# Performance work log

Hardware: AMD Instinct MI355X
Metric: run time of the kernel (lower is better)

The kernel has to match this reference:

```python
import jax, jax.numpy as jnp
import numpy as np

B, L, D, H = 4, 2048, 1024, 16
DH = D // H

def setup_inputs() -> dict:
    key = jax.random.key(0)
    ks = jax.random.split(key, 9)
    s = 1.0 / np.sqrt(D)
    x = jax.random.normal(ks[0], (B, L, D), dtype=jnp.float32)
    Wq = jax.random.uniform(ks[1], (D, D), jnp.float32, -s, s)
    bq = jax.random.uniform(ks[2], (D,), jnp.float32, -s, s)
    Wk = jax.random.uniform(ks[3], (D, D), jnp.float32, -s, s)
    bk = jax.random.uniform(ks[4], (D,), jnp.float32, -s, s)
    Wv = jax.random.uniform(ks[5], (D, D), jnp.float32, -s, s)
    bv = jax.random.uniform(ks[6], (D,), jnp.float32, -s, s)
    Wo = jax.random.uniform(ks[7], (D, D), jnp.float32, -s, s)
    bo = jax.random.uniform(ks[8], (D,), jnp.float32, -s, s)
    mask = jnp.tril(jnp.ones((L, L), dtype=jnp.int32))[None, None]  # [1,1,L,L] causal
    return {"x": x, "Wq": Wq, "bq": bq, "Wk": Wk, "bk": bk, "Wv": Wv, "bv": bv,
            "Wo": Wo, "bo": bo, "mask": mask}

def reference(x, Wq, bq, Wk, bk, Wv, bv, Wo, bo, mask):
    # projections (torch Linear: x @ W.T + b; here W stored transposed already as [D,D])
    q = (x @ Wq + bq).reshape(B, L, H, DH).transpose(0, 2, 1, 3)  # [B,H,L,Dh]
    k = (x @ Wk + bk).reshape(B, L, H, DH).transpose(0, 2, 1, 3)
    v = (x @ Wv + bv).reshape(B, L, H, DH).transpose(0, 2, 1, 3)
    scores = jnp.einsum('bhqd,bhkd->bhqk', q, k) / jnp.sqrt(jnp.float32(DH))
    scores = jnp.where(mask == 0, -jnp.inf, scores)
    attn = jax.nn.softmax(scores, axis=-1)
    out = jnp.einsum('bhqk,bhkd->bhqd', attn, v)  # [B,H,L,Dh]
    out = out.transpose(0, 2, 1, 3).reshape(B, L, D)
    return out @ Wo + bo
```

## Files before the change

kernel.cpp:

```cpp
#include <hip/hip_runtime.h>
#include <hip/hip_bf16.h>


typedef __bf16 bf16;
typedef __bf16 bf16x4 __attribute__((ext_vector_type(4)));
typedef __bf16 bf16x8 __attribute__((ext_vector_type(8)));
typedef float f32x4 __attribute__((ext_vector_type(4)));

#define DEV static __device__ __forceinline__

constexpr int B = 4, L = 2048, D = 1024, H = 16, DH = 64;
constexpr int BL = B * L;
constexpr int GM = 8192, GK = 1024;
constexpr int BKg = 64;

typedef __attribute__((address_space(1))) const void* gptr1;
typedef __attribute__((address_space(3))) void* lptr3;

DEV void load_lds16(const bf16* g, bf16* l) {
  __builtin_amdgcn_global_load_lds((gptr1)g, (lptr3)l, 16, 0, 0);
}

DEV f32x4 mfma(bf16x8 a, bf16x8 b, f32x4 c) {
  return __builtin_amdgcn_mfma_f32_16x16x32_bf16(a, b, c, 0, 0, 0);
}

DEV float scrub(float v) { return (v == v) ? v : 0.f; }
DEV float max3f(float a, float b, float c) { return fmaxf(fmaxf(a, b), c); }

__global__ void sniff_k(const unsigned short* __restrict__ xr, int* flag) {
  __shared__ int cnt;
  if (threadIdx.x == 0) cnt = 0;
  __syncthreads();
  int local = 0;
  for (int i = threadIdx.x; i < 4096; i += 256) {
    const unsigned short u = xr[2 * i];
    const int e = (u >> 7) & 0xFF;
    if (e >= 0x70 && e <= 0x85) local++;
  }
  atomicAdd(&cnt, local);
  __syncthreads();
  if (threadIdx.x == 0) *flag = (cnt > 2048) ? 1 : 0;
}

__global__ __launch_bounds__(256) void cvt_x_k(const void* __restrict__ src,
                                               bf16* __restrict__ dst,
                                               const int* __restrict__ flag, int n) {
  const bool isbf = (*flag != 0);
  const int stride = gridDim.x * blockDim.x * 8;
  for (int idx = (blockIdx.x * blockDim.x + threadIdx.x) * 8; idx < n; idx += stride) {
    bf16x8 o;
    if (isbf) {
      bf16x8 v = *(const bf16x8*)((const bf16*)src + idx);
      #pragma unroll
      for (int j = 0; j < 8; ++j) o[j] = (bf16)scrub((float)v[j]);
    } else {
      const float* s = (const float*)src + idx;
      #pragma unroll
      for (int j = 0; j < 8; ++j) o[j] = (bf16)scrub(s[j]);
    }
    *(bf16x8*)&dst[idx] = o;
  }
}

__global__ __launch_bounds__(256) void wtrans_cvt4_k(const void* __restrict__ W0,
                                                     const void* __restrict__ W1,
                                                     const void* __restrict__ W2,
                                                     const void* __restrict__ W3,
                                                     bf16* __restrict__ dstBase,
                                                     const int* __restrict__ flag) {
  __shared__ bf16 t[32][33];
  const bool isbf = (*flag != 0);
  const int z = blockIdx.z;
  const void* src = (z == 0) ? W0 : (z == 1) ? W1 : (z == 2) ? W2 : W3;
  bf16* dst = dstBase + (size_t)z * D * D;
  const int bx = blockIdx.x * 32, by = blockIdx.y * 32;
  const int tx = threadIdx.x & 31, ty = threadIdx.x >> 5;
  for (int i = ty; i < 32; i += 8) {
    const size_t off = (size_t)(by + i) * D + bx + tx;
    const float v = isbf ? (float)((const bf16*)src)[off] : ((const float*)src)[off];
    t[i][tx] = (bf16)scrub(v);
  }
  __syncthreads();
  for (int i = ty; i < 32; i += 8)
    dst[(size_t)(bx + i) * D + by + tx] = t[tx][i];
}

__global__ __launch_bounds__(256) void qkv_gemm_k(const bf16* __restrict__ A,
                                                  const bf16* __restrict__ Bt,
                                                  const void* __restrict__ bq,
                                                  const void* __restrict__ bk,
                                                  const void* __restrict__ bv,
                                                  bf16* __restrict__ Q,
                                                  bf16* __restrict__ Kk,
                                                  bf16* __restrict__ VT,
                                                  const int* __restrict__ flag) {
  __shared__ __align__(16) bf16 As[128 * BKg];
  __shared__ __align__(16) bf16 Bs[128 * BKg];
  const bool isbf = (*flag != 0);
  const int wg = blockIdx.x;
  const int local = wg >> 3;
  const int mt = (wg & 7) * 8 + (local & 7);
  const int nt = local >> 3;
  const int m0 = mt * 128, n0 = nt * 128;
  const int buf = n0 >> 10, nloc = n0 & 1023;
  const void* bias = (buf == 0) ? bq : (buf == 1) ? bk : bv;
  const float scale = (buf == 0) ? 0.18033688011111f : 1.0f;

  const int tid = threadIdx.x, wave = tid >> 6, lane = tid & 63;
  const int wr = wave >> 1, wc = wave & 1;
  const int quad = lane >> 4, l16 = lane & 15;
  const int srow = lane >> 3;
  const int scol = ((lane ^ srow) & 7) * 8;
  const int l7 = l16 & 7;
  const int s0 = ((quad ^ l7) * 8);
  const int s1 = s0 ^ 32;

  f32x4 acc[4][4] = {};

  for (int k0 = 0; k0 < GK; k0 += BKg) {
    for (int c = wave; c < 16; c += 4) {
      load_lds16(A  + (size_t)(m0 + c * 8 + srow) * GK + k0 + scol, &As[c * 512]);
      load_lds16(Bt + (size_t)(n0 + c * 8 + srow) * GK + k0 + scol, &Bs[c * 512]);
    }
    __syncthreads();
    #pragma unroll
    for (int kk = 0; kk < BKg; kk += 32) {
      const int sk = kk ? s1 : s0;
      bf16x8 af[4], bfr[4];
      #pragma unroll
      for (int i = 0; i < 4; ++i)
        af[i] = *(const bf16x8*)&As[(wr * 64 + i * 16 + l16) * BKg + sk];
      #pragma unroll
      for (int i = 0; i < 4; ++i)
        bfr[i] = *(const bf16x8*)&Bs[(wc * 64 + i * 16 + l16) * BKg + sk];
      #pragma unroll
      for (int mi = 0; mi < 4; ++mi)
        #pragma unroll
        for (int ni = 0; ni < 4; ++ni)
          acc[mi][ni] = mfma(af[mi], bfr[ni], acc[mi][ni]);
    }
    __syncthreads();
  }

  if (buf < 2) {
    bf16* Cb = (buf == 0) ? Q : Kk;
    #pragma unroll
    for (int ni = 0; ni < 4; ++ni) {
      const int col = nloc + wc * 64 + ni * 16 + l16;
      const float bv2 = isbf ? (float)((const bf16*)bias)[col] : ((const float*)bias)[col];
      #pragma unroll
      for (int mi = 0; mi < 4; ++mi)
        #pragma unroll
        for (int r = 0; r < 4; ++r) {
          const int row = m0 + wr * 64 + mi * 16 + quad * 4 + r;
          Cb[(size_t)row * D + col] = (bf16)((acc[mi][ni][r] + bv2) * scale);
        }
    }
  } else {
    #pragma unroll
    for (int ni = 0; ni < 4; ++ni) {
      const int col = nloc + wc * 64 + ni * 16 + l16;
      const int h = col >> 6, d = col & 63;
      const float bv2 = isbf ? (float)((const bf16*)bias)[col] : ((const float*)bias)[col];
      #pragma unroll
      for (int mi = 0; mi < 4; ++mi) {
        const int row = m0 + wr * 64 + mi * 16 + quad * 4;
        const int bb = row >> 11, l = row & 2047;
        const int pos = (l & ~31) + 4 * ((l >> 4) & 1) + 8 * ((l >> 2) & 3);
        bf16x4 pk;
        #pragma unroll
        for (int r = 0; r < 4; ++r) pk[r] = (bf16)(acc[mi][ni][r] + bv2);
        *(bf16x4*)&VT[((size_t)(bb * 16 + h) * 64 + d) * L + pos] = pk;
      }
    }
  }
}

__global__ __launch_bounds__(256) void gemm_bt_k(const bf16* __restrict__ A,
                                                 const bf16* __restrict__ Bt,
                                                 const void* __restrict__ bias,
                                                 void* __restrict__ C,
                                                 const int* __restrict__ flag) {
  __shared__ __align__(16) bf16 As[128 * BKg];
  __shared__ __align__(16) bf16 Bs[128 * BKg];
  const bool isbf = (*flag != 0);
  const int wg = blockIdx.x;
  const int local = wg >> 3;
  const int mt = (wg & 7) * 8 + (local & 7);
  const int nt = local >> 3;
  const int m0 = mt * 128, n0 = nt * 128;
  const int tid = threadIdx.x, wave = tid >> 6, lane = tid & 63;
  const int wr = wave >> 1, wc = wave & 1;
  const int quad = lane >> 4, l16 = lane & 15;
  const int srow = lane >> 3;
  const int scol = ((lane ^ srow) & 7) * 8;
  const int l7 = l16 & 7;
  const int s0 = ((quad ^ l7) * 8);
  const int s1 = s0 ^ 32;

  f32x4 acc[4][4] = {};

  for (int k0 = 0; k0 < GK; k0 += BKg) {
    for (int c = wave; c < 16; c += 4) {
      load_lds16(A  + (size_t)(m0 + c * 8 + srow) * GK + k0 + scol, &As[c * 512]);
      load_lds16(Bt + (size_t)(n0 + c * 8 + srow) * GK + k0 + scol, &Bs[c * 512]);
    }
    __syncthreads();
    #pragma unroll
    for (int kk = 0; kk < BKg; kk += 32) {
      const int sk = kk ? s1 : s0;
      bf16x8 af[4], bfr[4];
      #pragma unroll
      for (int i = 0; i < 4; ++i)
        af[i] = *(const bf16x8*)&As[(wr * 64 + i * 16 + l16) * BKg + sk];
      #pragma unroll
      for (int i = 0; i < 4; ++i)
        bfr[i] = *(const bf16x8*)&Bs[(wc * 64 + i * 16 + l16) * BKg + sk];
      #pragma unroll
      for (int mi = 0; mi < 4; ++mi)
        #pragma unroll
        for (int ni = 0; ni < 4; ++ni)
          acc[mi][ni] = mfma(af[mi], bfr[ni], acc[mi][ni]);
    }
    __syncthreads();
  }

  bf16* Cb = (bf16*)C;
  float* Cf = (float*)C;
  #pragma unroll
  for (int ni = 0; ni < 4; ++ni) {
    const int col = n0 + wc * 64 + ni * 16 + l16;
    const float bv = isbf ? (float)((const bf16*)bias)[col] : ((const float*)bias)[col];
    #pragma unroll
    for (int mi = 0; mi < 4; ++mi)
      #pragma unroll
      for (int r = 0; r < 4; ++r) {
        const int row = m0 + wr * 64 + mi * 16 + quad * 4 + r;
        const float v = acc[mi][ni][r] + bv;
        if (isbf) Cb[(size_t)row * D + col] = (bf16)v;
        else      Cf[(size_t)row * D + col] = v;
      }
  }
}

__global__ __launch_bounds__(256) void attn_k(bf16* QO,
                                              const bf16* __restrict__ K,
                                              const bf16* __restrict__ VT) {
  __shared__ __align__(16) bf16 Ks[2][64 * 64];
  __shared__ __align__(16) bf16 Vt[2][64 * 64];

  const int bx = blockIdx.x;
  const int qt = (L / 64 - 1) - (bx >> 6);
  const int bh = bx & 63;
  const int b = bh >> 4, h = bh & 15;
  const int tid = threadIdx.x, wave = tid >> 6, lane = tid & 63;
  const int quad = lane >> 4, l16 = lane & 15;
  const int srow = lane >> 3;
  const int scol = ((lane ^ srow) & 7) * 8;
  const int l7 = l16 & 7;
  const int s0 = ((quad ^ l7) * 8);
  const int s1 = s0 ^ 32;

  bf16* Qb = QO + (size_t)b * L * D + h * DH;
  const bf16* Kb = K + (size_t)b * L * D + h * DH;
  const bf16* VTg = VT + (size_t)bh * DH * L;

  const int qrow = qt * 64 + wave * 16 + l16;
  const bf16x8 qf0 = *(const bf16x8*)(Qb + (size_t)qrow * D + quad * 8);
  const bf16x8 qf1 = *(const bf16x8*)(Qb + (size_t)qrow * D + 32 + quad * 8);

  bf16x8 ones;
  #pragma unroll
  for (int j = 0; j < 8; ++j) ones[j] = (bf16)1.0f;

  float m_run = -INFINITY;
  f32x4 o_acc[4] = {};
  f32x4 o_sum = {};

  const int nkt = qt + 1;

  const bf16* kg0 = Kb + (size_t)(wave * 8 + srow) * D + scol;
  const bf16* kg1 = kg0 + (size_t)32 * D;
  const bf16* vg0 = VTg + (size_t)(wave * 8 + srow) * L + scol;
  const bf16* vg1 = vg0 + (size_t)32 * L;
  const int kl0 = wave * 512, kl1 = kl0 + 2048;

  load_lds16(kg0, &Ks[0][kl0]);
  load_lds16(kg1, &Ks[0][kl1]);
  load_lds16(vg0, &Vt[0][kl0]);
  load_lds16(vg1, &Vt[0][kl1]);
  kg0 += (size_t)64 * D; kg1 += (size_t)64 * D; vg0 += 64; vg1 += 64;
  __syncthreads();

  int cur = 0;
  for (int kt = 0; kt < nkt; ++kt) {
    if (kt + 1 < nkt) {
      bf16* Kn = &Ks[cur ^ 1][0];
      bf16* Vn = &Vt[cur ^ 1][0];
      load_lds16(kg0, &Kn[kl0]);
      load_lds16(kg1, &Kn[kl1]);
      load_lds16(vg0, &Vn[kl0]);
      load_lds16(vg1, &Vn[kl1]);
      kg0 += (size_t)64 * D; kg1 += (size_t)64 * D; vg0 += 64; vg1 += 64;
    }

    const bf16* Kc = &Ks[cur][0];
    const bf16* Vc = &Vt[cur][0];

    f32x4 s[4];
    #pragma unroll
    for (int sub = 0; sub < 4; ++sub) {
      bf16x8 k0 = *(const bf16x8*)&Kc[(sub * 16 + l16) * 64 + s0];
      bf16x8 k1 = *(const bf16x8*)&Kc[(sub * 16 + l16) * 64 + s1];
      f32x4 a = {};
      a = mfma(k0, qf0, a);
      a = mfma(k1, qf1, a);
      s[sub] = a;
    }

    if (kt == qt) {
      const int qloc = wave * 16 + l16;
      #pragma unroll
      for (int sub = 0; sub < 4; ++sub)
        #pragma unroll
        for (int r = 0; r < 4; ++r)
          if (sub * 16 + quad * 4 + r > qloc) s[sub][r] = -1e30f;
    }

    const float t0 = max3f(s[0][0], s[0][1], s[0][2]);
    const float t1 = max3f(s[0][3], s[1][0], s[1][1]);
    const float t2 = max3f(s[1][2], s[1][3], s[2][0]);
    const float t3 = max3f(s[2][1], s[2][2], s[2][3]);
    const float t4 = max3f(s[3][0], s[3][1], s[3][2]);
    float mx = fmaxf(max3f(t0, t1, t2), max3f(t3, t4, s[3][3]));
    mx = fmaxf(mx, __shfl_xor(mx, 16, 64));
    mx = fmaxf(mx, __shfl_xor(mx, 32, 64));

    if (!__all(mx <= m_run + 8.f)) {
      const float mn = fmaxf(m_run, mx);
      const float alpha = __builtin_amdgcn_exp2f(m_run - mn);
      m_run = mn;
      #pragma unroll
      for (int r = 0; r < 4; ++r) {
        const float ar = __shfl(alpha, quad * 4 + r, 64);
        o_sum[r] *= ar;
        #pragma unroll
        for (int db = 0; db < 4; ++db) o_acc[db][r] *= ar;
      }
    }

    bf16x8 fr0, fr1;
    #pragma unroll
    for (int r = 0; r < 4; ++r) {
      fr0[r]     = (bf16)__builtin_amdgcn_exp2f(s[0][r] - m_run);
      fr0[4 + r] = (bf16)__builtin_amdgcn_exp2f(s[1][r] - m_run);
      fr1[r]     = (bf16)__builtin_amdgcn_exp2f(s[2][r] - m_run);
      fr1[4 + r] = (bf16)__builtin_amdgcn_exp2f(s[3][r] - m_run);
    }

    o_sum = mfma(fr0, ones, o_sum);
    o_sum = mfma(fr1, ones, o_sum);
    #pragma unroll
    for (int db = 0; db < 4; ++db) {
      bf16x8 v0 = *(const bf16x8*)&Vc[(db * 16 + l16) * 64 + s0];
      bf16x8 v1 = *(const bf16x8*)&Vc[(db * 16 + l16) * 64 + s1];
      o_acc[db] = mfma(fr0, v0, o_acc[db]);
      o_acc[db] = mfma(fr1, v1, o_acc[db]);
    }

    __syncthreads();
    cur ^= 1;
  }

  #pragma unroll
  for (int r = 0; r < 4; ++r) {
    const float inv = 1.f / o_sum[r];
    const int row = qt * 64 + wave * 16 + quad * 4 + r;
    #pragma unroll
    for (int db = 0; db < 4; ++db)
      Qb[(size_t)row * D + db * 16 + l16] = (bf16)(o_acc[db][r] * inv);
  }
}

extern "C" void kernel_launch(void* const* d_in, const int* in_sizes, int n_in,
                              void* d_out, int out_size, void* d_ws, size_t ws_size,
                              hipStream_t stream) {
  const void* x  = d_in[0];
  const void* Wq = d_in[1];
  const void* bq = d_in[2];
  const void* Wk = d_in[3];
  const void* bk = d_in[4];
  const void* Wv = d_in[5];
  const void* bv = d_in[6];
  const void* Wo = d_in[7];
  const void* bo = d_in[8];

  int* flag = (int*)d_ws;
  char* p = (char*)d_ws + 4096;
  bf16* xc  = (bf16*)p;                 p += (size_t)BL * D * 2;
  bf16* WqT = (bf16*)p;                 p += (size_t)D * D * 2;
  bf16* WkT = (bf16*)p;                 p += (size_t)D * D * 2;
  bf16* WvT = (bf16*)p;                 p += (size_t)D * D * 2;
  bf16* WoT = (bf16*)p;                 p += (size_t)D * D * 2;
  bf16* Qb  = (bf16*)p;                 p += (size_t)BL * D * 2;
  bf16* Kb  = (bf16*)p;                 p += (size_t)BL * D * 2;
  bf16* VTb = (bf16*)p;

  sniff_k<<<1, 256, 0, stream>>>((const unsigned short*)x, flag);

  cvt_x_k<<<1024, 256, 0, stream>>>(x, xc, flag, BL * D);
  wtrans_cvt4_k<<<dim3(32, 32, 4), 256, 0, stream>>>(Wq, Wk, Wv, Wo, WqT, flag);

  qkv_gemm_k<<<dim3(1536), 256, 0, stream>>>(
      xc, WqT, bq, bk, bv, Qb, Kb, VTb, flag);

  attn_k<<<dim3((L / 64) * B * H), 256, 0, stream>>>(Qb, Kb, VTb);

  gemm_bt_k<<<dim3(512), 256, 0, stream>>>(Qb, WoT, bo, d_out, flag);
}
```

Measured before the change: 267.6 us.

## Process two query tiles per attention block and simplify GEMM grid mapping

The attention kernel now handles 128 query rows per block as two 64-row sub-tiles. Each K/V tile is loaded into LDS once and reused for both sub-tiles, which halves K/V traffic per query and doubles MFMA work between barriers. The trade-off is more registers per thread and fewer blocks, so the causal load imbalance between blocks gets coarser. The GEMM kernels also drop the swizzled 1D block-to-tile mapping in favour of a plain 2D grid, which may reduce L2 locality.

```diff
diff --git a/kernel.cpp b/kernel.cpp
--- a/kernel.cpp
+++ b/kernel.cpp
@@ -98,11 +98,7 @@
   __shared__ __align__(16) bf16 As[128 * BKg];
   __shared__ __align__(16) bf16 Bs[128 * BKg];
   const bool isbf = (*flag != 0);
-  const int wg = blockIdx.x;
-  const int local = wg >> 3;
-  const int mt = (wg & 7) * 8 + (local & 7);
-  const int nt = local >> 3;
-  const int m0 = mt * 128, n0 = nt * 128;
+  const int m0 = blockIdx.x * 128, n0 = blockIdx.y * 128;
   const int buf = n0 >> 10, nloc = n0 & 1023;
   const void* bias = (buf == 0) ? bq : (buf == 1) ? bk : bv;
   const float scale = (buf == 0) ? 0.18033688011111f : 1.0f;
@@ -185,11 +181,7 @@
   __shared__ __align__(16) bf16 As[128 * BKg];
   __shared__ __align__(16) bf16 Bs[128 * BKg];
   const bool isbf = (*flag != 0);
-  const int wg = blockIdx.x;
-  const int local = wg >> 3;
-  const int mt = (wg & 7) * 8 + (local & 7);
-  const int nt = local >> 3;
-  const int m0 = mt * 128, n0 = nt * 128;
+  const int m0 = blockIdx.x * 128, n0 = blockIdx.y * 128;
   const int tid = threadIdx.x, wave = tid >> 6, lane = tid & 63;
   const int wr = wave >> 1, wc = wave & 1;
   const int quad = lane >> 4, l16 = lane & 15;
@@ -251,7 +243,7 @@
   __shared__ __align__(16) bf16 Vt[2][64 * 64];
 
   const int bx = blockIdx.x;
-  const int qt = (L / 64 - 1) - (bx >> 6);
+  const int qt = (L / 128 - 1) - (bx >> 6);
   const int bh = bx & 63;
   const int b = bh >> 4, h = bh & 15;
   const int tid = threadIdx.x, wave = tid >> 6, lane = tid & 63;
@@ -266,19 +258,23 @@
   const bf16* Kb = K + (size_t)b * L * D + h * DH;
   const bf16* VTg = VT + (size_t)bh * DH * L;
 
-  const int qrow = qt * 64 + wave * 16 + l16;
-  const bf16x8 qf0 = *(const bf16x8*)(Qb + (size_t)qrow * D + quad * 8);
-  const bf16x8 qf1 = *(const bf16x8*)(Qb + (size_t)qrow * D + 32 + quad * 8);
+  bf16x8 qf[2][2];
+  #pragma unroll
+  for (int sq = 0; sq < 2; ++sq) {
+    const int qrow = qt * 128 + sq * 64 + wave * 16 + l16;
+    qf[sq][0] = *(const bf16x8*)(Qb + (size_t)qrow * D + quad * 8);
+    qf[sq][1] = *(const bf16x8*)(Qb + (size_t)qrow * D + 32 + quad * 8);
+  }
 
   bf16x8 ones;
   #pragma unroll
   for (int j = 0; j < 8; ++j) ones[j] = (bf16)1.0f;
 
-  float m_run = -INFINITY;
-  f32x4 o_acc[4] = {};
-  f32x4 o_sum = {};
-
-  const int nkt = qt + 1;
+  float m_run[2] = {-INFINITY, -INFINITY};
+  f32x4 o_acc[2][4] = {};
+  f32x4 o_sum[2] = {};
+
+  const int nkt = 2 * qt + 2;
 
   const bf16* kg0 = Kb + (size_t)(wave * 8 + srow) * D + scol;
   const bf16* kg1 = kg0 + (size_t)32 * D;
@@ -308,65 +304,78 @@
     const bf16* Kc = &Ks[cur][0];
     const bf16* Vc = &Vt[cur][0];
 
-    f32x4 s[4];
+    bf16x8 kf0[4], kf1[4];
     #pragma unroll
     for (int sub = 0; sub < 4; ++sub) {
-      bf16x8 k0 = *(const bf16x8*)&Kc[(sub * 16 + l16) * 64 + s0];
-      bf16x8 k1 = *(const bf16x8*)&Kc[(sub * 16 + l16) * 64 + s1];
-      f32x4 a = {};
-      a = mfma(k0, qf0, a);
-      a = mfma(k1, qf1, a);
-      s[sub] = a;
-    }
-
-    if (kt == qt) {
-      const int qloc = wave * 16 + l16;
-      #pragma unroll
-      for (int sub = 0; sub < 4; ++sub)
-        #pragma unroll
-        for (int r = 0; r < 4; ++r)
-          if (sub * 16 + quad * 4 + r > qloc) s[sub][r] = -1e30f;
-    }
-
-    const float t0 = max3f(s[0][0], s[0][1], s[0][2]);
-    const float t1 = max3f(s[0][3], s[1][0], s[1][1]);
-    const float t2 = max3f(s[1][2], s[1][3], s[2][0]);
-    const float t3 = max3f(s[2][1], s[2][2], s[2][3]);
-    const float t4 = max3f(s[3][0], s[3][1], s[3][2]);
-    float mx = fmaxf(max3f(t0, t1, t2), max3f(t3, t4, s[3][3]));
-    mx = fmaxf(mx, __shfl_xor(mx, 16, 64));
-    mx = fmaxf(mx, __shfl_xor(mx, 32, 64));
-
-    if (!__all(mx <= m_run + 8.f)) {
-      const float mn = fmaxf(m_run, mx);
-      const float alpha = __builtin_amdgcn_exp2f(m_run - mn);
-      m_run = mn;
+      kf0[sub] = *(const bf16x8*)&Kc[(sub * 16 + l16) * 64 + s0];
+      kf1[sub] = *(const bf16x8*)&Kc[(sub * 16 + l16) * 64 + s1];
+    }
+
+    f32x4 sv[2][4];
+    #pragma unroll
+    for (int sq = 0; sq < 2; ++sq)
+      #pragma unroll
+      for (int sub = 0; sub < 4; ++sub) {
+        f32x4 a = {};
+        a = mfma(kf0[sub], qf[sq][0], a);
+        a = mfma(kf1[sub], qf[sq][1], a);
+        sv[sq][sub] = a;
+      }
+
+    bf16x8 fr[2][2];
+    #pragma unroll
+    for (int sq = 0; sq < 2; ++sq) {
+      if (kt >= 2 * qt + sq) {
+        const int qloc = (2 * qt + sq - kt) * 64 + wave * 16 + l16;
+        #pragma unroll
+        for (int sub = 0; sub < 4; ++sub)
+          #pragma unroll
+          for (int r = 0; r < 4; ++r)
+            if (sub * 16 + quad * 4 + r > qloc) sv[sq][sub][r] = -1e30f;
+      }
+
+      const float t0 = max3f(sv[sq][0][0], sv[sq][0][1], sv[sq][0][2]);
+      const float t1 = max3f(sv[sq][0][3], sv[sq][1][0], sv[sq][1][1]);
+      const float t2 = max3f(sv[sq][1][2], sv[sq][1][3], sv[sq][2][0]);
+      const float t3 = max3f(sv[sq][2][1], sv[sq][2][2], sv[sq][2][3]);
+      const float t4 = max3f(sv[sq][3][0], sv[sq][3][1], sv[sq][3][2]);
+      float mx = fmaxf(max3f(t0, t1, t2), max3f(t3, t4, sv[sq][3][3]));
+      mx = fmaxf(mx, __shfl_xor(mx, 16, 64));
+      mx = fmaxf(mx, __shfl_xor(mx, 32, 64));
+
+      if (!__all(mx <= m_run[sq] + 8.f)) {
+        const float mn = fmaxf(m_run[sq], mx);
+        const float alpha = __builtin_amdgcn_exp2f(m_run[sq] - mn);
+        m_run[sq] = mn;
+        #pragma unroll
+        for (int r = 0; r < 4; ++r) {
+          const float ar = __shfl(alpha, quad * 4 + r, 64);
+          o_sum[sq][r] *= ar;
+          #pragma unroll
+          for (int db = 0; db < 4; ++db) o_acc[sq][db][r] *= ar;
+        }
+      }
+
       #pragma unroll
       for (int r = 0; r < 4; ++r) {
-        const float ar = __shfl(alpha, quad * 4 + r, 64);
-        o_sum[r] *= ar;
-        #pragma unroll
-        for (int db = 0; db < 4; ++db) o_acc[db][r] *= ar;
-      }
-    }
-
-    bf16x8 fr0, fr1;
-    #pragma unroll
-    for (int r = 0; r < 4; ++r) {
-      fr0[r]     = (bf16)__builtin_amdgcn_exp2f(s[0][r] - m_run);
-      fr0[4 + r] = (bf16)__builtin_amdgcn_exp2f(s[1][r] - m_run);
-      fr1[r]     = (bf16)__builtin_amdgcn_exp2f(s[2][r] - m_run);
-      fr1[4 + r] = (bf16)__builtin_amdgcn_exp2f(s[3][r] - m_run);
-    }
-
-    o_sum = mfma(fr0, ones, o_sum);
-    o_sum = mfma(fr1, ones, o_sum);
+        fr[sq][0][r]     = (bf16)__builtin_amdgcn_exp2f(sv[sq][0][r] - m_run[sq]);
+        fr[sq][0][4 + r] = (bf16)__builtin_amdgcn_exp2f(sv[sq][1][r] - m_run[sq]);
+        fr[sq][1][r]     = (bf16)__builtin_amdgcn_exp2f(sv[sq][2][r] - m_run[sq]);
+        fr[sq][1][4 + r] = (bf16)__builtin_amdgcn_exp2f(sv[sq][3][r] - m_run[sq]);
+      }
+
+      o_sum[sq] = mfma(fr[sq][0], ones, o_sum[sq]);
+      o_sum[sq] = mfma(fr[sq][1], ones, o_sum[sq]);
+    }
+
     #pragma unroll
     for (int db = 0; db < 4; ++db) {
       bf16x8 v0 = *(const bf16x8*)&Vc[(db * 16 + l16) * 64 + s0];
       bf16x8 v1 = *(const bf16x8*)&Vc[(db * 16 + l16) * 64 + s1];
-      o_acc[db] = mfma(fr0, v0, o_acc[db]);
-      o_acc[db] = mfma(fr1, v1, o_acc[db]);
+      o_acc[0][db] = mfma(fr[0][0], v0, o_acc[0][db]);
+      o_acc[0][db] = mfma(fr[0][1], v1, o_acc[0][db]);
+      o_acc[1][db] = mfma(fr[1][0], v0, o_acc[1][db]);
+      o_acc[1][db] = mfma(fr[1][1], v1, o_acc[1][db]);
     }
 
     __syncthreads();
@@ -374,13 +383,15 @@
   }
 
   #pragma unroll
-  for (int r = 0; r < 4; ++r) {
-    const float inv = 1.f / o_sum[r];
-    const int row = qt * 64 + wave * 16 + quad * 4 + r;
-    #pragma unroll
-    for (int db = 0; db < 4; ++db)
-      Qb[(size_t)row * D + db * 16 + l16] = (bf16)(o_acc[db][r] * inv);
-  }
+  for (int sq = 0; sq < 2; ++sq)
+    #pragma unroll
+    for (int r = 0; r < 4; ++r) {
+      const float inv = 1.f / o_sum[sq][r];
+      const int row = qt * 128 + sq * 64 + wave * 16 + quad * 4 + r;
+      #pragma unroll
+      for (int db = 0; db < 4; ++db)
+        Qb[(size_t)row * D + db * 16 + l16] = (bf16)(o_acc[sq][db][r] * inv);
+    }
 }
 
 extern "C" void kernel_launch(void* const* d_in, const int* in_sizes, int n_in,
@@ -412,10 +423,10 @@
   cvt_x_k<<<1024, 256, 0, stream>>>(x, xc, flag, BL * D);
   wtrans_cvt4_k<<<dim3(32, 32, 4), 256, 0, stream>>>(Wq, Wk, Wv, Wo, WqT, flag);
 
-  qkv_gemm_k<<<dim3(1536), 256, 0, stream>>>(
+  qkv_gemm_k<<<dim3(GM / 128, 3072 / 128), 256, 0, stream>>>(
       xc, WqT, bq, bk, bv, Qb, Kb, VTb, flag);
 
-  attn_k<<<dim3((L / 64) * B * H), 256, 0, stream>>>(Qb, Kb, VTb);
-
-  gemm_bt_k<<<dim3(512), 256, 0, stream>>>(Qb, WoT, bo, d_out, flag);
-}
+  attn_k<<<dim3((L / 128) * B * H), 256, 0, stream>>>(Qb, Kb, VTb);
+
+  gemm_bt_k<<<dim3(GM / 128, D / 128), 256, 0, stream>>>(Qb, WoT, bo, d_out, flag);
+}
```

Measured after the change: 268.5 us. About the same (+0.3%).
